# Optimization experiments

Hardware: AMD Instinct MI355X
Metric: run time of the kernel (lower is better)

The kernel has to match this reference:

```python
import jax, jax.numpy as jnp
import numpy as np
import math

B, S, D, H, L, DFF = 64, 512, 512, 8, 2, 1024
DK = D // H
NEG = -1e32
LN_EPS = 1e-5


def cosine_pos_emb(seqlen, d_model):
    # pe[:,0::2]=sin(pos*div), pe[:,1::2]=cos(pos*div) -- fully overwrites the randn init
    pos = jnp.arange(seqlen, dtype=jnp.float32)[:, None]
    div = jnp.exp(jnp.arange(0, d_model, 2, dtype=jnp.float32) * (-math.log(10000.0) / d_model))
    ang = pos * div  # [S, D/2]
    return jnp.stack([jnp.sin(ang), jnp.cos(ang)], axis=-1).reshape(seqlen, d_model)


def layernorm(x, g, b):
    m = jnp.mean(x, axis=-1, keepdims=True)
    v = jnp.var(x, axis=-1, keepdims=True)
    return g * (x - m) * jax.lax.rsqrt(v + LN_EPS) + b


def setup_inputs() -> dict:
    key = jax.random.key(0)
    ks = jax.random.split(key, 8)
    sc = 0.02
    inp = {
        'q_embed_data': jax.random.normal(ks[0], (B, S, D), jnp.float32),
        'qa_embed_data': jax.random.normal(ks[1], (B, S, D), jnp.float32),
        'forget_rate': jax.random.uniform(ks[2], (B, 1, S, 1), jnp.float32),
        # per-block params, leading dim = n_blocks (kq_same=1: q uses k_linear)
        'Wk': jax.random.normal(ks[3], (L, D, D), jnp.float32) * sc,
        'bk': jnp.zeros((L, D), jnp.float32),
        'Wv': jax.random.normal(ks[4], (L, D, D), jnp.float32) * sc,
        'bv': jnp.zeros((L, D), jnp.float32),
        'Wo': jax.random.normal(ks[5], (L, D, D), jnp.float32) * sc,
        'bo': jnp.zeros((L, D), jnp.float32),
        'ln1_g': jnp.ones((L, D), jnp.float32),
        'ln1_b': jnp.zeros((L, D), jnp.float32),
        'W1': jax.random.normal(ks[6], (L, D, DFF), jnp.float32) * sc,
        'b1': jnp.zeros((L, DFF), jnp.float32),
        'W2': jax.random.normal(ks[7], (L, DFF, D), jnp.float32) * sc,
        'b2': jnp.zeros((L, D), jnp.float32),
        'ln2_g': jnp.ones((L, D), jnp.float32),
        'ln2_b': jnp.zeros((L, D), jnp.float32),
    }
    return inp


def reference(q_embed_data, qa_embed_data, forget_rate, Wk, bk, Wv, bv, Wo, bo,
              ln1_g, ln1_b, W1, b1, W2, b2, ln2_g, ln2_b):
    pe = cosine_pos_emb(S, D)
    x = q_embed_data + pe  # query/key stream
    y = qa_embed_data + pe  # value stream (fixed across blocks)
    # mask=0 path: np.triu(ones, k=0) == 0 -> strictly lower-triangular allowed
    allow = jnp.tril(jnp.ones((S, S), dtype=bool), -1)
    scale = 1.0 / math.sqrt(DK)
    for i in range(L):
        qk = (x @ Wk[i] + bk[i]).reshape(B, S, H, DK).transpose(0, 2, 1, 3)  # [B,H,S,dk]
        v = (y @ Wv[i] + bv[i]).reshape(B, S, H, DK).transpose(0, 2, 1, 3)
        scores = jnp.einsum('bhqd,bhkd->bhqk', qk, qk) * scale
        scores = scores * forget_rate  # [B,1,S,1] broadcasts over heads and keys
        scores = jnp.where(allow, scores, NEG)
        p = jax.nn.softmax(scores, axis=-1)
        p = p.at[:, :, 0, :].set(0.0)  # zero_pad: first query row zeroed
        attn = jnp.einsum('bhqk,bhkd->bhqd', p, v).transpose(0, 2, 1, 3).reshape(B, S, D)
        attn = attn @ Wo[i] + bo[i]
        x = layernorm(x + attn, ln1_g[i], ln1_b[i])
        ff = jax.nn.relu(x @ W1[i] + b1[i]) @ W2[i] + b2[i]
        x = layernorm(x + ff, ln2_g[i], ln2_b[i])
    return x
```

## Files before the change

### kernel.cpp

```cpp
#include <hip/hip_runtime.h>
#include <cstdio>

#define B_   64
#define S_   512
#define D_   512
#define H_   8
#define DK_  64
#define DFF_ 1024
#define L_   2
#define BS_  (B_ * S_)

typedef __attribute__((ext_vector_type(8))) short bf16x8;
typedef __attribute__((ext_vector_type(4))) short bf16x4;
typedef __attribute__((ext_vector_type(4))) float f32x4;

__device__ inline short f2bf(float f) {
  unsigned u = __float_as_uint(f);
  u = u + 0x7FFF + ((u >> 16) & 1);
  return (short)(u >> 16);
}
__device__ inline float bf2f(short s) {
  return __uint_as_float(((unsigned)(unsigned short)s) << 16);
}

__device__ inline void gl_lds16(const short* g, void* lds_base) {
  __builtin_amdgcn_global_load_lds(
      (const __attribute__((address_space(1))) void*)g,
      (__attribute__((address_space(3))) void*)lds_base, 16, 0, 0);
}

__global__ void pe_kernel(float* __restrict__ pe) {
  int idx = blockIdx.x * 256 + threadIdx.x;
  int s = idx >> 9, d = idx & 511;
  float dv = __expf((float)(d & ~1) * (-9.210340371976184f / (float)D_));
  float ang = (float)s * dv;
  pe[idx] = (d & 1) ? cosf(ang) : sinf(ang);
}

__global__ __launch_bounds__(256) void prep_kernel(
    const float* __restrict__ q, const float* __restrict__ qa,
    const float* __restrict__ pe,
    short* __restrict__ xb, short* __restrict__ yb) {
  size_t base = ((size_t)blockIdx.x * 256 + threadIdx.x) * 8;
  int sd = (int)(base & (size_t)(S_ * D_ - 1));
  f32x4 p0 = *(const f32x4*)(pe + sd);
  f32x4 p1 = *(const f32x4*)(pe + sd + 4);
  f32x4 q0 = *(const f32x4*)(q + base);
  f32x4 q1 = *(const f32x4*)(q + base + 4);
  f32x4 a0 = *(const f32x4*)(qa + base);
  f32x4 a1 = *(const f32x4*)(qa + base + 4);
  bf16x8 xv, yv;
#pragma unroll
  for (int i = 0; i < 4; ++i) {
    xv[i] = f2bf(q0[i] + p0[i]);
    yv[i] = f2bf(a0[i] + p0[i]);
  }
#pragma unroll
  for (int i = 0; i < 4; ++i) {
    xv[4 + i] = f2bf(q1[i] + p1[i]);
    yv[4 + i] = f2bf(a1[i] + p1[i]);
  }
  *(bf16x8*)(xb + base) = xv;
  *(bf16x8*)(yb + base) = yv;
}

struct TrArgs {
  const float* src[10];
  short* dst[10];
  int R[10], C[10];
};
__global__ __launch_bounds__(256) void tr_w_all(TrArgs a) {
  const int slot = blockIdx.z;
  const int R = a.R[slot], C = a.C[slot];
  const int c0 = blockIdx.x * 64, r0 = blockIdx.y * 64;
  if (c0 >= C || r0 >= R) return;
  const float* __restrict__ src = a.src[slot];
  short* __restrict__ dst = a.dst[slot];
  __shared__ short Ts[64][72];
  const int t = threadIdx.x;
#pragma unroll
  for (int it = 0; it < 2; ++it) {
    int c2 = it * 256 + t;
    int srow = c2 >> 3, schunk = c2 & 7;
    const float* sp = src + (size_t)(r0 + srow) * C + c0 + schunk * 8;
    f32x4 a0 = *(const f32x4*)sp;
    f32x4 a1 = *(const f32x4*)(sp + 4);
#pragma unroll
    for (int k = 0; k < 4; ++k) Ts[srow][schunk * 8 + k] = f2bf(a0[k]);
#pragma unroll
    for (int k = 0; k < 4; ++k) Ts[srow][schunk * 8 + 4 + k] = f2bf(a1[k]);
  }
  __syncthreads();
#pragma unroll
  for (int it = 0; it < 2; ++it) {
    int c2 = it * 256 + t;
    int orow = c2 >> 3, ochunk = c2 & 7;
    bf16x8 vv;
#pragma unroll
    for (int k = 0; k < 8; ++k) vv[k] = Ts[ochunk * 8 + k][orow];
    *(bf16x8*)(dst + (size_t)(c0 + orow) * R + r0 + ochunk * 8) = vv;
  }
}

__global__ __launch_bounds__(256, 2) void gemm_bt(
    const short* __restrict__ A, const short* __restrict__ BT,
    const float* __restrict__ bias, short* __restrict__ Cb,
    int M, int N, int K, int relu, int bias_row, int nx, int xmaj)
{
  const int nwg = gridDim.x;
  const int cpx = nwg >> 3;
  const int l = (blockIdx.x & 7) * cpx + (blockIdx.x >> 3);
  int bcol, brow;
  if (xmaj) { bcol = l % nx; brow = l / nx; }
  else      { int ny = nwg / nx; brow = l % ny; bcol = l / ny; }

  __shared__ __align__(16) short As[2][128][32];
  __shared__ __align__(16) short Bs[2][256][32];
  const int t = threadIdx.x;
  const int w = t >> 6, lane = t & 63, lr = lane & 15, lk = lane >> 4;
  const int wr = w >> 1, wc = w & 1;

  const f32x4 vzero = {0.f, 0.f, 0.f, 0.f};
  f32x4 acc[4][8];
#pragma unroll
  for (int m = 0; m < 4; ++m)
#pragma unroll
    for (int n = 0; n < 8; ++n) acc[m][n] = vzero;

  const short* Abase = A + (size_t)brow * 128 * K;
  const short* Bbase = BT + (size_t)bcol * 256 * K;

  auto stage = [&](int buf, int k0) {
#pragma unroll
    for (int it = 0; it < 2; ++it) {
      int cb = it * 256 + w * 64;
      int c = cb + lane;
      gl_lds16(Abase + (size_t)(c >> 2) * K + k0 + (c & 3) * 8, (char*)&As[buf][0][0] + (size_t)cb * 16);
    }
#pragma unroll
    for (int it = 0; it < 4; ++it) {
      int cb = it * 256 + w * 64;
      int c = cb + lane;
      gl_lds16(Bbase + (size_t)(c >> 2) * K + k0 + (c & 3) * 8, (char*)&Bs[buf][0][0] + (size_t)cb * 16);
    }
  };

  stage(0, 0);
  int cur = 0;
  for (int k0 = 0; k0 < K; k0 += 32) {
    if (k0 + 32 < K) {
      stage(cur ^ 1, k0 + 32);
      asm volatile("s_waitcnt vmcnt(6)" ::: "memory");
    } else {
      asm volatile("s_waitcnt vmcnt(0)" ::: "memory");
    }
    asm volatile("s_barrier" ::: "memory");

    bf16x8 af[4], bf[8];
#pragma unroll
    for (int m = 0; m < 4; ++m) af[m] = *(const bf16x8*)&As[cur][wr * 64 + m * 16 + lr][lk * 8];
#pragma unroll
    for (int n = 0; n < 8; ++n) bf[n] = *(const bf16x8*)&Bs[cur][wc * 128 + n * 16 + lr][lk * 8];
#pragma unroll
    for (int m = 0; m < 4; ++m)
#pragma unroll
      for (int n = 0; n < 8; ++n)
        acc[m][n] = __builtin_amdgcn_mfma_f32_16x16x32_bf16(bf[n], af[m], acc[m][n], 0, 0, 0);

    asm volatile("s_barrier" ::: "memory");
    cur ^= 1;
  }

#pragma unroll
  for (int m = 0; m < 4; ++m) {
    int row = brow * 128 + wr * 64 + m * 16 + lr;
    float brv = (bias && bias_row) ? bias[row] : 0.f;
    size_t rb = (size_t)row * N;
#pragma unroll
    for (int n = 0; n < 8; ++n) {
      int colb = bcol * 256 + wc * 128 + n * 16 + lk * 4;
      f32x4 bv4;
      if (bias && !bias_row) bv4 = *(const f32x4*)(bias + colb);
      else { bv4[0] = brv; bv4[1] = brv; bv4[2] = brv; bv4[3] = brv; }
      bf16x4 ov;
#pragma unroll
      for (int j = 0; j < 4; ++j) {
        float vv = acc[m][n][j] + bv4[j];
        if (relu) vv = fmaxf(vv, 0.f);
        ov[j] = f2bf(vv);
      }
      *(bf16x4*)(Cb + rb + colb) = ov;
    }
  }
}

template<int P>
__device__ __forceinline__ void attn_body(
    const short* __restrict__ qk, const short* __restrict__ vT,
    const float* __restrict__ fr, short* __restrict__ out,
    short (*Pl)[552], float (*redsum)[32][4],
    int h, int b, int w, int lr, int lk)
{
  constexpr int qo0 = 32 * P, qo1 = 32 * (15 - P);
  constexpr int c0 = 2 * P + 2;
  constexpr int colb1 = c0 * 16;
  constexpr int n0 = P + 1;
  constexpr int n1 = 16 - P;

  const size_t qk_head = (size_t)b * S_ * D_ + (size_t)h * DK_;
  const float scale = 0.125f;

  bf16x8 qf0[2][2], qf1[2][2];
#pragma unroll
  for (int qt = 0; qt < 2; ++qt)
#pragma unroll
    for (int ks = 0; ks < 2; ++ks) {
      qf0[qt][ks] = *(const bf16x8*)(qk + qk_head + (size_t)(qo0 + qt * 16 + lr) * D_ + ks * 32 + lk * 8);
      qf1[qt][ks] = *(const bf16x8*)(qk + qk_head + (size_t)(qo1 + qt * 16 + lr) * D_ + ks * 32 + lk * 8);
    }

  float frv0[2], frv1[2];
#pragma unroll
  for (int qt = 0; qt < 2; ++qt) {
    frv0[qt] = scale * fr[(size_t)b * S_ + qo0 + qt * 16 + lr];
    frv1[qt] = scale * fr[(size_t)b * S_ + qo1 + qt * 16 + lr];
  }

  const f32x4 vzero = {0.f, 0.f, 0.f, 0.f};
  f32x4 acc[9][2];
#pragma unroll
  for (int i = 0; i < 9; ++i) { acc[i][0] = vzero; acc[i][1] = vzero; }

  const int nfr = (w < 2) ? 9 : 8;
  const short* kqbase = qk + qk_head + (size_t)lr * D_ + lk * 8;
  auto kfoff = [&](int i) -> size_t {
    int f = w + 4 * i;
    int kt = (f < c0) ? f : f - c0;
    return (size_t)kt * 16 * D_;
  };
  bf16x8 kbuf[2][2];
  {
    const short* p = kqbase + kfoff(0);
    kbuf[0][0] = *(const bf16x8*)p;
    kbuf[0][1] = *(const bf16x8*)(p + 32);
  }
#pragma unroll
  for (int i = 0; i < 9; ++i) {
    if (i < nfr) {
      if (i + 1 < nfr) {
        const short* p = kqbase + kfoff(i + 1);
        kbuf[(i + 1) & 1][0] = *(const bf16x8*)p;
        kbuf[(i + 1) & 1][1] = *(const bf16x8*)(p + 32);
      }
      __builtin_amdgcn_sched_barrier(0);
      const int f = w + 4 * i;
      if (f < c0) {
#pragma unroll
        for (int ks = 0; ks < 2; ++ks) {
          acc[i][0] = __builtin_amdgcn_mfma_f32_16x16x32_bf16(kbuf[i & 1][ks], qf0[0][ks], acc[i][0], 0, 0, 0);
          acc[i][1] = __builtin_amdgcn_mfma_f32_16x16x32_bf16(kbuf[i & 1][ks], qf0[1][ks], acc[i][1], 0, 0, 0);
        }
      } else {
#pragma unroll
        for (int ks = 0; ks < 2; ++ks) {
          acc[i][0] = __builtin_amdgcn_mfma_f32_16x16x32_bf16(kbuf[i & 1][ks], qf1[0][ks], acc[i][0], 0, 0, 0);
          acc[i][1] = __builtin_amdgcn_mfma_f32_16x16x32_bf16(kbuf[i & 1][ks], qf1[1][ks], acc[i][1], 0, 0, 0);
        }
      }
      __builtin_amdgcn_sched_barrier(0);
    }
  }

  const int uqt0 = w & 1, udh0 = w >> 1;
  const int uqt1 = w >> 1, udh1 = w & 1;
  const short* vu0 = vT + (size_t)(h * DK_ + udh0 * 32 + lr) * BS_ + (size_t)b * S_ + lk * 8;
  const short* vu1 = vT + (size_t)(h * DK_ + udh1 * 32 + lr) * BS_ + (size_t)b * S_ + lk * 8;
  bf16x8 vfB[2][2][2];
#pragma unroll
  for (int n = 0; n < 2; ++n) {
    vfB[0][0][n] = *(const bf16x8*)(vu0 + (size_t)n * 16 * BS_);
    vfB[0][1][n] = *(const bf16x8*)(vu1 + (size_t)n * 16 * BS_);
  }
  if (1 < n0) {
#pragma unroll
    for (int n = 0; n < 2; ++n)
      vfB[1][0][n] = *(const bf16x8*)(vu0 + (size_t)n * 16 * BS_ + 32);
  }
#pragma unroll
  for (int n = 0; n < 2; ++n)
    vfB[1][1][n] = *(const bf16x8*)(vu1 + (size_t)n * 16 * BS_ + 32);
  __builtin_amdgcn_sched_barrier(0);

  float rs00 = 0.f, rs01 = 0.f, rs10 = 0.f, rs11 = 0.f;
#pragma unroll
  for (int frag = 0; frag < 34; ++frag) {
    if ((frag & 3) == w) {
      const int i = frag >> 2;
      const int tl = (frag < c0) ? 0 : 1;
      const int kt = tl ? frag - c0 : frag;
      const int kbase = kt * 16 + lk * 4;
      const int colb = (tl ? colb1 : 0) + kbase;
#pragma unroll
      for (int qt = 0; qt < 2; ++qt) {
        int qrow = (tl ? qo1 : qo0) + qt * 16 + lr;
        float fv = tl ? frv1[qt] : frv0[qt];
        bf16x4 pk;
        float rs = 0.f;
#pragma unroll
        for (int j = 0; j < 4; ++j) {
          float e = (kbase + j < qrow) ? __expf(acc[i][qt][j] * fv) : 0.f;
          rs += e;
          pk[j] = f2bf(e);
        }
        *(bf16x4*)&Pl[qt * 16 + lr][colb] = pk;
        if (tl == 0) { if (qt == 0) rs00 += rs; else rs01 += rs; }
        else         { if (qt == 0) rs10 += rs; else rs11 += rs; }
      }
    }
  }

#pragma unroll
  for (int msk = 16; msk < 64; msk <<= 1) {
    rs00 += __shfl_xor(rs00, msk);
    rs01 += __shfl_xor(rs01, msk);
    rs10 += __shfl_xor(rs10, msk);
    rs11 += __shfl_xor(rs11, msk);
  }
  if (lk == 0) {
    redsum[0][lr][w] = rs00;
    redsum[0][16 + lr][w] = rs01;
    redsum[1][lr][w] = rs10;
    redsum[1][16 + lr][w] = rs11;
  }
  __syncthreads();

  const short* prow0 = &Pl[uqt0 * 16 + lr][lk * 8];
  const short* prow1 = &Pl[uqt1 * 16 + lr][colb1 + lk * 8];
  f32x4 oacc0[2] = {vzero, vzero}, oacc1[2] = {vzero, vzero};
  bf16x8 paB[2][2];
  paB[0][0] = *(const bf16x8*)prow0;
  paB[0][1] = *(const bf16x8*)prow1;

#pragma unroll
  for (int kb = 0; kb < 16; ++kb) {
    const int pc = kb & 1, pn = pc ^ 1;
    if (kb + 1 < n0) paB[pn][0] = *(const bf16x8*)(prow0 + (kb + 1) * 32);
    if (kb + 1 < n1) paB[pn][1] = *(const bf16x8*)(prow1 + (kb + 1) * 32);
    __builtin_amdgcn_sched_barrier(0);
    if (kb < n0) {
#pragma unroll
      for (int n = 0; n < 2; ++n)
        oacc0[n] = __builtin_amdgcn_mfma_f32_16x16x32_bf16(paB[pc][0], vfB[pc][0][n], oacc0[n], 0, 0, 0);
    }
    if (kb < n1) {
#pragma unroll
      for (int n = 0; n < 2; ++n)
        oacc1[n] = __builtin_amdgcn_mfma_f32_16x16x32_bf16(paB[pc][1], vfB[pc][1][n], oacc1[n], 0, 0, 0);
    }
    __builtin_amdgcn_sched_barrier(0);
    if (kb + 2 < n0) {
#pragma unroll
      for (int n = 0; n < 2; ++n)
        vfB[pc][0][n] = *(const bf16x8*)(vu0 + (size_t)n * 16 * BS_ + (kb + 2) * 32);
    }
    if (kb + 2 < n1) {
#pragma unroll
      for (int n = 0; n < 2; ++n)
        vfB[pc][1][n] = *(const bf16x8*)(vu1 + (size_t)n * 16 * BS_ + (kb + 2) * 32);
    }
    __builtin_amdgcn_sched_barrier(0);
  }

  {
    float invd[4];
#pragma unroll
    for (int j = 0; j < 4; ++j) {
      int row = uqt0 * 16 + lk * 4 + j;
      float ds = redsum[0][row][0] + redsum[0][row][1] + redsum[0][row][2] + redsum[0][row][3];
      invd[j] = ds > 0.f ? 1.f / ds : 0.f;
    }
#pragma unroll
    for (int n = 0; n < 2; ++n)
#pragma unroll
      for (int j = 0; j < 4; ++j) {
        int qrow = qo0 + uqt0 * 16 + lk * 4 + j;
        out[qk_head + (size_t)qrow * D_ + udh0 * 32 + n * 16 + lr] = f2bf(oacc0[n][j] * invd[j]);
      }
  }
  {
    float invd[4];
#pragma unroll
    for (int j = 0; j < 4; ++j) {
      int row = uqt1 * 16 + lk * 4 + j;
      float ds = redsum[1][row][0] + redsum[1][row][1] + redsum[1][row][2] + redsum[1][row][3];
      invd[j] = ds > 0.f ? 1.f / ds : 0.f;
    }
#pragma unroll
    for (int n = 0; n < 2; ++n)
#pragma unroll
      for (int j = 0; j < 4; ++j) {
        int qrow = qo1 + uqt1 * 16 + lk * 4 + j;
        out[qk_head + (size_t)qrow * D_ + udh1 * 32 + n * 16 + lr] = f2bf(oacc1[n][j] * invd[j]);
      }
  }
}

__global__ __launch_bounds__(256, 3) void attn_kernel(
    const short* __restrict__ qk, const short* __restrict__ vT,
    const float* __restrict__ fr, short* __restrict__ out)
{
  const int hw = blockIdx.x;
  const int l = (hw & 7) * 512 + (hw >> 3);
  const int p = l & 7, hb = l >> 3;
  const int h = hb & 7, b = hb >> 3;
  const int t = threadIdx.x;
  const int w = t >> 6, lr = t & 15, lk = (t & 63) >> 4;

  __shared__ short Pl[32][552];
  __shared__ float redsum[2][32][4];

  switch (p) {
    case 0: attn_body<0>(qk, vT, fr, out, Pl, redsum, h, b, w, lr, lk); break;
    case 1: attn_body<1>(qk, vT, fr, out, Pl, redsum, h, b, w, lr, lk); break;
    case 2: attn_body<2>(qk, vT, fr, out, Pl, redsum, h, b, w, lr, lk); break;
    case 3: attn_body<3>(qk, vT, fr, out, Pl, redsum, h, b, w, lr, lk); break;
    case 4: attn_body<4>(qk, vT, fr, out, Pl, redsum, h, b, w, lr, lk); break;
    case 5: attn_body<5>(qk, vT, fr, out, Pl, redsum, h, b, w, lr, lk); break;
    case 6: attn_body<6>(qk, vT, fr, out, Pl, redsum, h, b, w, lr, lk); break;
    case 7: attn_body<7>(qk, vT, fr, out, Pl, redsum, h, b, w, lr, lk); break;
  }
}

template<int FINAL>
__global__ __launch_bounds__(256) void ln_res_t(
    const short* __restrict__ xin, const short* __restrict__ add,
    const float* __restrict__ g, const float* __restrict__ bb,
    short* __restrict__ xbout, float* __restrict__ fout)
{
  const int row = blockIdx.x * 4 + (threadIdx.x >> 6);
  const int lane = threadIdx.x & 63;
  const size_t base = (size_t)row * D_ + lane * 8;

  bf16x8 xv = *(const bf16x8*)(xin + base);
  bf16x8 av = *(const bf16x8*)(add + base);
  float vals[8];
#pragma unroll
  for (int i = 0; i < 8; ++i) vals[i] = bf2f(xv[i]) + bf2f(av[i]);

  float s = 0.f, sq = 0.f;
#pragma unroll
  for (int i = 0; i < 8; ++i) { s += vals[i]; sq += vals[i] * vals[i]; }
#pragma unroll
  for (int m = 1; m < 64; m <<= 1) { s += __shfl_xor(s, m); sq += __shfl_xor(sq, m); }

  float mean = s * (1.f / D_);
  float var = sq * (1.f / D_) - mean * mean;
  float rstd = rsqrtf(var + 1e-5f);

  int col = lane * 8;
  if (FINAL) {
    f32x4 o0, o1;
#pragma unroll
    for (int i = 0; i < 8; ++i) {
      float vv = g[col + i] * (vals[i] - mean) * rstd + bb[col + i];
      if (i < 4) o0[i] = vv; else o1[i - 4] = vv;
    }
    *(f32x4*)(fout + base) = o0;
    *(f32x4*)(fout + base + 4) = o1;
  } else {
    bf16x8 ob;
#pragma unroll
    for (int i = 0; i < 8; ++i)
      ob[i] = f2bf(g[col + i] * (vals[i] - mean) * rstd + bb[col + i]);
    *(bf16x8*)(xbout + base) = ob;
  }
}

extern "C" void kernel_launch(void* const* d_in, const int* in_sizes, int n_in,
                              void* d_out, int out_size, void* d_ws, size_t ws_size,
                              hipStream_t stream) {
  const float* q_emb = (const float*)d_in[0];
  const float* qa_emb = (const float*)d_in[1];
  const float* frate = (const float*)d_in[2];
  const float* Wk = (const float*)d_in[3];
  const float* bk = (const float*)d_in[4];
  const float* Wv = (const float*)d_in[5];
  const float* bv = (const float*)d_in[6];
  const float* Wo = (const float*)d_in[7];
  const float* bo = (const float*)d_in[8];
  const float* ln1g = (const float*)d_in[9];
  const float* ln1b = (const float*)d_in[10];
  const float* W1 = (const float*)d_in[11];
  const float* b1 = (const float*)d_in[12];
  const float* W2 = (const float*)d_in[13];
  const float* b2 = (const float*)d_in[14];
  const float* ln2g = (const float*)d_in[15];
  const float* ln2b = (const float*)d_in[16];
  float* x = (float*)d_out;

  char* ws = (char*)d_ws;
  size_t off = 0;
  auto alloc = [&](size_t bytes) -> void* {
    void* p = ws + off;
    off += (bytes + 255) & ~(size_t)255;
    return p;
  };
  const size_t MTOK = (size_t)BS_;
  float* pe    = (float*)alloc((size_t)S_ * D_ * 4);
  short* xb    = (short*)alloc(MTOK * D_ * 2);
  short* yb    = (short*)alloc(MTOK * D_ * 2);
  short* qkb   = (short*)alloc(MTOK * D_ * 2);
  short* vTb   = (short*)alloc(MTOK * D_ * 2);
  short* ff1b  = (short*)alloc(MTOK * DFF_ * 2);
  short* attnb = ff1b;
  short* goutb = qkb;
  short* wT[L_][5];
  for (int i = 0; i < L_; ++i) {
    wT[i][0] = (short*)alloc((size_t)D_ * D_ * 2);
    wT[i][1] = (short*)alloc((size_t)D_ * D_ * 2);
    wT[i][2] = (short*)alloc((size_t)D_ * D_ * 2);
    wT[i][3] = (short*)alloc((size_t)D_ * DFF_ * 2);
    wT[i][4] = (short*)alloc((size_t)DFF_ * D_ * 2);
  }
  if (off > ws_size) {
    fprintf(stderr, "parKT: workspace overflow: need %zu have %zu\n", off, ws_size);
    return;
  }

  pe_kernel<<<(S_ * D_) / 256, 256, 0, stream>>>(pe);
  prep_kernel<<<(int)(MTOK * D_ / (256 * 8)), 256, 0, stream>>>(q_emb, qa_emb, pe, xb, yb);

  TrArgs ta;
  for (int i = 0; i < L_; ++i) {
    ta.src[i * 5 + 0] = Wk + (size_t)i * D_ * D_;  ta.dst[i * 5 + 0] = wT[i][0]; ta.R[i * 5 + 0] = D_;   ta.C[i * 5 + 0] = D_;
    ta.src[i * 5 + 1] = Wv + (size_t)i * D_ * D_;  ta.dst[i * 5 + 1] = wT[i][1]; ta.R[i * 5 + 1] = D_;   ta.C[i * 5 + 1] = D_;
    ta.src[i * 5 + 2] = Wo + (size_t)i * D_ * D_;  ta.dst[i * 5 + 2] = wT[i][2]; ta.R[i * 5 + 2] = D_;   ta.C[i * 5 + 2] = D_;
    ta.src[i * 5 + 3] = W1 + (size_t)i * D_ * DFF_; ta.dst[i * 5 + 3] = wT[i][3]; ta.R[i * 5 + 3] = D_;   ta.C[i * 5 + 3] = DFF_;
    ta.src[i * 5 + 4] = W2 + (size_t)i * DFF_ * D_; ta.dst[i * 5 + 4] = wT[i][4]; ta.R[i * 5 + 4] = DFF_; ta.C[i * 5 + 4] = D_;
  }
  tr_w_all<<<dim3(DFF_ / 64, DFF_ / 64, 10), 256, 0, stream>>>(ta);

  const int M = (int)MTOK;
  for (int i = 0; i < L_; ++i) {
    gemm_bt<<<(M / 128) * (D_ / 256), 256, 0, stream>>>(xb, wT[i][0], bk + (size_t)i * D_, qkb, M, D_, D_, 0, 0, D_ / 256, 1);
    gemm_bt<<<(D_ / 128) * (M / 256), 256, 0, stream>>>(wT[i][1], yb, bv + (size_t)i * D_, vTb, D_, M, D_, 0, 1, M / 256, 0);
    attn_kernel<<<(S_ / 64) * H_ * B_, 256, 0, stream>>>(qkb, vTb, frate, attnb);
    gemm_bt<<<(M / 128) * (D_ / 256), 256, 0, stream>>>(attnb, wT[i][2], bo + (size_t)i * D_, goutb, M, D_, D_, 0, 0, D_ / 256, 1);
    ln_res_t<0><<<M / 4, 256, 0, stream>>>(xb, goutb, ln1g + (size_t)i * D_, ln1b + (size_t)i * D_, xb, nullptr);
    gemm_bt<<<(M / 128) * (DFF_ / 256), 256, 0, stream>>>(xb, wT[i][3], b1 + (size_t)i * DFF_, ff1b, M, DFF_, D_, 1, 0, DFF_ / 256, 1);
    gemm_bt<<<(M / 128) * (D_ / 256), 256, 0, stream>>>(ff1b, wT[i][4], b2 + (size_t)i * D_, goutb, M, D_, DFF_, 0, 0, D_ / 256, 1);
    if (i == L_ - 1)
      ln_res_t<1><<<M / 4, 256, 0, stream>>>(xb, goutb, ln2g + (size_t)i * D_, ln2b + (size_t)i * D_, nullptr, x);
    else
      ln_res_t<0><<<M / 4, 256, 0, stream>>>(xb, goutb, ln2g + (size_t)i * D_, ln2b + (size_t)i * D_, xb, nullptr);
  }
}
```

Baseline: 730.0 us.

## Split attention block work across eight waves instead of four

The attention kernel now launches 512 threads per block, so eight waves share the QK^T fragments and the PV output tiles. Each wave handles half as many score fragments and exactly one output tile, and the row-sum reduction array grows to eight partial sums. The explicit double-buffered K/V/P prefetch with sched_barriers is dropped in favour of simple per-iteration loads. This aims to add latency hiding through more waves, but it loses the hand-built software pipelining and raises per-CU thread pressure.

```diff
diff --git a/kernel.cpp b/kernel.cpp
--- a/kernel.cpp
+++ b/kernel.cpp
@@ -198,7 +198,7 @@
 __device__ __forceinline__ void attn_body(
     const short* __restrict__ qk, const short* __restrict__ vT,
     const float* __restrict__ fr, short* __restrict__ out,
-    short (*Pl)[552], float (*redsum)[32][4],
+    short (*Pl)[552], float (*redsum)[32][8],
     int h, int b, int w, int lr, int lk)
 {
   constexpr int qo0 = 32 * P, qo1 = 32 * (15 - P);
@@ -227,77 +227,41 @@
   }
 
   const f32x4 vzero = {0.f, 0.f, 0.f, 0.f};
-  f32x4 acc[9][2];
-#pragma unroll
-  for (int i = 0; i < 9; ++i) { acc[i][0] = vzero; acc[i][1] = vzero; }
-
-  const int nfr = (w < 2) ? 9 : 8;
-  const short* kqbase = qk + qk_head + (size_t)lr * D_ + lk * 8;
-  auto kfoff = [&](int i) -> size_t {
-    int f = w + 4 * i;
-    int kt = (f < c0) ? f : f - c0;
-    return (size_t)kt * 16 * D_;
-  };
-  bf16x8 kbuf[2][2];
-  {
-    const short* p = kqbase + kfoff(0);
-    kbuf[0][0] = *(const bf16x8*)p;
-    kbuf[0][1] = *(const bf16x8*)(p + 32);
-  }
-#pragma unroll
-  for (int i = 0; i < 9; ++i) {
+  const int nfr = (w < 2) ? 5 : 4;
+
+  f32x4 acc[5][2];
+#pragma unroll
+  for (int i = 0; i < 5; ++i) { acc[i][0] = vzero; acc[i][1] = vzero; }
+
+#pragma unroll
+  for (int i = 0; i < 5; ++i) {
     if (i < nfr) {
-      if (i + 1 < nfr) {
-        const short* p = kqbase + kfoff(i + 1);
-        kbuf[(i + 1) & 1][0] = *(const bf16x8*)p;
-        kbuf[(i + 1) & 1][1] = *(const bf16x8*)(p + 32);
+      const int f = w + 8 * i;
+      const int kt = (f < c0) ? f : f - c0;
+      const short* kp = qk + qk_head + (size_t)(kt * 16 + lr) * D_ + lk * 8;
+      bf16x8 kf0 = *(const bf16x8*)kp;
+      bf16x8 kf1 = *(const bf16x8*)(kp + 32);
+      if (f < c0) {
+        acc[i][0] = __builtin_amdgcn_mfma_f32_16x16x32_bf16(kf0, qf0[0][0], acc[i][0], 0, 0, 0);
+        acc[i][0] = __builtin_amdgcn_mfma_f32_16x16x32_bf16(kf1, qf0[0][1], acc[i][0], 0, 0, 0);
+        acc[i][1] = __builtin_amdgcn_mfma_f32_16x16x32_bf16(kf0, qf0[1][0], acc[i][1], 0, 0, 0);
+        acc[i][1] = __builtin_amdgcn_mfma_f32_16x16x32_bf16(kf1, qf0[1][1], acc[i][1], 0, 0, 0);
+      } else {
+        acc[i][0] = __builtin_amdgcn_mfma_f32_16x16x32_bf16(kf0, qf1[0][0], acc[i][0], 0, 0, 0);
+        acc[i][0] = __builtin_amdgcn_mfma_f32_16x16x32_bf16(kf1, qf1[0][1], acc[i][0], 0, 0, 0);
+        acc[i][1] = __builtin_amdgcn_mfma_f32_16x16x32_bf16(kf0, qf1[1][0], acc[i][1], 0, 0, 0);
+        acc[i][1] = __builtin_amdgcn_mfma_f32_16x16x32_bf16(kf1, qf1[1][1], acc[i][1], 0, 0, 0);
       }
-      __builtin_amdgcn_sched_barrier(0);
-      const int f = w + 4 * i;
-      if (f < c0) {
-#pragma unroll
-        for (int ks = 0; ks < 2; ++ks) {
-          acc[i][0] = __builtin_amdgcn_mfma_f32_16x16x32_bf16(kbuf[i & 1][ks], qf0[0][ks], acc[i][0], 0, 0, 0);
-          acc[i][1] = __builtin_amdgcn_mfma_f32_16x16x32_bf16(kbuf[i & 1][ks], qf0[1][ks], acc[i][1], 0, 0, 0);
-        }
-      } else {
-#pragma unroll
-        for (int ks = 0; ks < 2; ++ks) {
-          acc[i][0] = __builtin_amdgcn_mfma_f32_16x16x32_bf16(kbuf[i & 1][ks], qf1[0][ks], acc[i][0], 0, 0, 0);
-          acc[i][1] = __builtin_amdgcn_mfma_f32_16x16x32_bf16(kbuf[i & 1][ks], qf1[1][ks], acc[i][1], 0, 0, 0);
-        }
-      }
-      __builtin_amdgcn_sched_barrier(0);
-    }
-  }
-
-  const int uqt0 = w & 1, udh0 = w >> 1;
-  const int uqt1 = w >> 1, udh1 = w & 1;
-  const short* vu0 = vT + (size_t)(h * DK_ + udh0 * 32 + lr) * BS_ + (size_t)b * S_ + lk * 8;
-  const short* vu1 = vT + (size_t)(h * DK_ + udh1 * 32 + lr) * BS_ + (size_t)b * S_ + lk * 8;
-  bf16x8 vfB[2][2][2];
-#pragma unroll
-  for (int n = 0; n < 2; ++n) {
-    vfB[0][0][n] = *(const bf16x8*)(vu0 + (size_t)n * 16 * BS_);
-    vfB[0][1][n] = *(const bf16x8*)(vu1 + (size_t)n * 16 * BS_);
-  }
-  if (1 < n0) {
-#pragma unroll
-    for (int n = 0; n < 2; ++n)
-      vfB[1][0][n] = *(const bf16x8*)(vu0 + (size_t)n * 16 * BS_ + 32);
-  }
-#pragma unroll
-  for (int n = 0; n < 2; ++n)
-    vfB[1][1][n] = *(const bf16x8*)(vu1 + (size_t)n * 16 * BS_ + 32);
-  __builtin_amdgcn_sched_barrier(0);
+    }
+  }
 
   float rs00 = 0.f, rs01 = 0.f, rs10 = 0.f, rs11 = 0.f;
 #pragma unroll
-  for (int frag = 0; frag < 34; ++frag) {
-    if ((frag & 3) == w) {
-      const int i = frag >> 2;
-      const int tl = (frag < c0) ? 0 : 1;
-      const int kt = tl ? frag - c0 : frag;
+  for (int i = 0; i < 5; ++i) {
+    if (i < nfr) {
+      const int f = w + 8 * i;
+      const int tl = (f < c0) ? 0 : 1;
+      const int kt = tl ? f - c0 : f;
       const int kbase = kt * 16 + lk * 4;
       const int colb = (tl ? colb1 : 0) + kbase;
 #pragma unroll
@@ -305,16 +269,16 @@
         int qrow = (tl ? qo1 : qo0) + qt * 16 + lr;
         float fv = tl ? frv1[qt] : frv0[qt];
         bf16x4 pk;
-        float rs = 0.f;
+        float rsl = 0.f;
 #pragma unroll
         for (int j = 0; j < 4; ++j) {
           float e = (kbase + j < qrow) ? __expf(acc[i][qt][j] * fv) : 0.f;
-          rs += e;
+          rsl += e;
           pk[j] = f2bf(e);
         }
         *(bf16x4*)&Pl[qt * 16 + lr][colb] = pk;
-        if (tl == 0) { if (qt == 0) rs00 += rs; else rs01 += rs; }
-        else         { if (qt == 0) rs10 += rs; else rs11 += rs; }
+        if (tl == 0) { if (qt == 0) rs00 += rsl; else rs01 += rsl; }
+        else         { if (qt == 0) rs10 += rsl; else rs11 += rsl; }
       }
     }
   }
@@ -334,78 +298,41 @@
   }
   __syncthreads();
 
-  const short* prow0 = &Pl[uqt0 * 16 + lr][lk * 8];
-  const short* prow1 = &Pl[uqt1 * 16 + lr][colb1 + lk * 8];
-  f32x4 oacc0[2] = {vzero, vzero}, oacc1[2] = {vzero, vzero};
-  bf16x8 paB[2][2];
-  paB[0][0] = *(const bf16x8*)prow0;
-  paB[0][1] = *(const bf16x8*)prow1;
-
-#pragma unroll
-  for (int kb = 0; kb < 16; ++kb) {
-    const int pc = kb & 1, pn = pc ^ 1;
-    if (kb + 1 < n0) paB[pn][0] = *(const bf16x8*)(prow0 + (kb + 1) * 32);
-    if (kb + 1 < n1) paB[pn][1] = *(const bf16x8*)(prow1 + (kb + 1) * 32);
-    __builtin_amdgcn_sched_barrier(0);
-    if (kb < n0) {
-#pragma unroll
-      for (int n = 0; n < 2; ++n)
-        oacc0[n] = __builtin_amdgcn_mfma_f32_16x16x32_bf16(paB[pc][0], vfB[pc][0][n], oacc0[n], 0, 0, 0);
-    }
-    if (kb < n1) {
-#pragma unroll
-      for (int n = 0; n < 2; ++n)
-        oacc1[n] = __builtin_amdgcn_mfma_f32_16x16x32_bf16(paB[pc][1], vfB[pc][1][n], oacc1[n], 0, 0, 0);
-    }
-    __builtin_amdgcn_sched_barrier(0);
-    if (kb + 2 < n0) {
-#pragma unroll
-      for (int n = 0; n < 2; ++n)
-        vfB[pc][0][n] = *(const bf16x8*)(vu0 + (size_t)n * 16 * BS_ + (kb + 2) * 32);
-    }
-    if (kb + 2 < n1) {
-#pragma unroll
-      for (int n = 0; n < 2; ++n)
-        vfB[pc][1][n] = *(const bf16x8*)(vu1 + (size_t)n * 16 * BS_ + (kb + 2) * 32);
-    }
-    __builtin_amdgcn_sched_barrier(0);
-  }
-
-  {
-    float invd[4];
+  const int ut = w >> 2, uqt = (w >> 1) & 1, udh = w & 1;
+  const int nu = ut ? n1 : n0;
+  const int colbu = ut ? colb1 : 0;
+  const int qo = ut ? qo1 : qo0;
+  const short* vu = vT + (size_t)(h * DK_ + udh * 32 + lr) * BS_ + (size_t)b * S_ + lk * 8;
+  const short* prow = &Pl[uqt * 16 + lr][colbu + lk * 8];
+
+  f32x4 oacc[2] = {vzero, vzero};
+  for (int kb = 0; kb < nu; ++kb) {
+    bf16x8 pa = *(const bf16x8*)(prow + kb * 32);
+    bf16x8 v0 = *(const bf16x8*)(vu + kb * 32);
+    bf16x8 v1 = *(const bf16x8*)(vu + (size_t)16 * BS_ + kb * 32);
+    oacc[0] = __builtin_amdgcn_mfma_f32_16x16x32_bf16(pa, v0, oacc[0], 0, 0, 0);
+    oacc[1] = __builtin_amdgcn_mfma_f32_16x16x32_bf16(pa, v1, oacc[1], 0, 0, 0);
+  }
+
+  float invd[4];
+#pragma unroll
+  for (int j = 0; j < 4; ++j) {
+    int row = uqt * 16 + lk * 4 + j;
+    float ds = 0.f;
+#pragma unroll
+    for (int c = 0; c < 8; ++c) ds += redsum[ut][row][c];
+    invd[j] = ds > 0.f ? 1.f / ds : 0.f;
+  }
+#pragma unroll
+  for (int n = 0; n < 2; ++n)
 #pragma unroll
     for (int j = 0; j < 4; ++j) {
-      int row = uqt0 * 16 + lk * 4 + j;
-      float ds = redsum[0][row][0] + redsum[0][row][1] + redsum[0][row][2] + redsum[0][row][3];
-      invd[j] = ds > 0.f ? 1.f / ds : 0.f;
-    }
-#pragma unroll
-    for (int n = 0; n < 2; ++n)
-#pragma unroll
-      for (int j = 0; j < 4; ++j) {
-        int qrow = qo0 + uqt0 * 16 + lk * 4 + j;
-        out[qk_head + (size_t)qrow * D_ + udh0 * 32 + n * 16 + lr] = f2bf(oacc0[n][j] * invd[j]);
-      }
-  }
-  {
-    float invd[4];
-#pragma unroll
-    for (int j = 0; j < 4; ++j) {
-      int row = uqt1 * 16 + lk * 4 + j;
-      float ds = redsum[1][row][0] + redsum[1][row][1] + redsum[1][row][2] + redsum[1][row][3];
-      invd[j] = ds > 0.f ? 1.f / ds : 0.f;
-    }
-#pragma unroll
-    for (int n = 0; n < 2; ++n)
-#pragma unroll
-      for (int j = 0; j < 4; ++j) {
-        int qrow = qo1 + uqt1 * 16 + lk * 4 + j;
-        out[qk_head + (size_t)qrow * D_ + udh1 * 32 + n * 16 + lr] = f2bf(oacc1[n][j] * invd[j]);
-      }
-  }
-}
-
-__global__ __launch_bounds__(256, 3) void attn_kernel(
+      int qrow = qo + uqt * 16 + lk * 4 + j;
+      out[qk_head + (size_t)qrow * D_ + udh * 32 + n * 16 + lr] = f2bf(oacc[n][j] * invd[j]);
+    }
+}
+
+__global__ __launch_bounds__(512, 4) void attn_kernel(
     const short* __restrict__ qk, const short* __restrict__ vT,
     const float* __restrict__ fr, short* __restrict__ out)
 {
@@ -416,8 +343,8 @@
   const int t = threadIdx.x;
   const int w = t >> 6, lr = t & 15, lk = (t & 63) >> 4;
 
-  __shared__ short Pl[32][552];
-  __shared__ float redsum[2][32][4];
+  __shared__ __align__(16) short Pl[32][552];
+  __shared__ __align__(16) float redsum[2][32][8];
 
   switch (p) {
     case 0: attn_body<0>(qk, vT, fr, out, Pl, redsum, h, b, w, lr, lk); break;
@@ -544,7 +471,7 @@
   for (int i = 0; i < L_; ++i) {
     gemm_bt<<<(M / 128) * (D_ / 256), 256, 0, stream>>>(xb, wT[i][0], bk + (size_t)i * D_, qkb, M, D_, D_, 0, 0, D_ / 256, 1);
     gemm_bt<<<(D_ / 128) * (M / 256), 256, 0, stream>>>(wT[i][1], yb, bv + (size_t)i * D_, vTb, D_, M, D_, 0, 1, M / 256, 0);
-    attn_kernel<<<(S_ / 64) * H_ * B_, 256, 0, stream>>>(qkb, vTb, frate, attnb);
+    attn_kernel<<<(S_ / 64) * H_ * B_, 512, 0, stream>>>(qkb, vTb, frate, attnb);
     gemm_bt<<<(M / 128) * (D_ / 256), 256, 0, stream>>>(attnb, wT[i][2], bo + (size_t)i * D_, goutb, M, D_, D_, 0, 0, D_ / 256, 1);
     ln_res_t<0><<<M / 4, 256, 0, stream>>>(xb, goutb, ln1g + (size_t)i * D_, ln1b + (size_t)i * D_, xb, nullptr);
     gemm_bt<<<(M / 128) * (DFF_ / 256), 256, 0, stream>>>(xb, wT[i][3], b1 + (size_t)i * DFF_, ff1b, M, DFF_, D_, 1, 0, DFF_ / 256, 1);
```

Measured after the change: 755.2 us. 1.03x slower.
